# Optimization experiments

Measured on AMD Instinct MI355X. Metric: run time of the kernel, lower is better.

The kernel has to match this reference:

```python
import jax, jax.numpy as jnp
import numpy as np

N_NODES = 50000
N_EDGES = 800000
D_IN = 128
D_HID = 128
D_OUT = 128


def setup_inputs() -> dict:
    key = jax.random.key(0)
    ks = jax.random.split(key, 6)
    x = jax.random.normal(ks[0], (N_NODES, D_IN), dtype=jnp.float32)
    edge_index = jax.random.randint(ks[1], (2, N_EDGES), 0, N_NODES, dtype=jnp.int64)
    s_in = 1.0 / np.sqrt(D_IN)
    s_hid = 1.0 / np.sqrt(D_HID)
    W1 = jax.random.normal(ks[2], (D_IN, D_HID), dtype=jnp.float32) * s_in
    b1 = jnp.zeros((D_HID,), dtype=jnp.float32)
    W2 = jax.random.normal(ks[3], (D_HID, D_OUT), dtype=jnp.float32) * s_hid
    b2 = jnp.zeros((D_OUT,), dtype=jnp.float32)
    return {"x": x, "edge_index": edge_index, "W1": W1, "b1": b1, "W2": W2, "b2": b2}


def gcn_conv(x, src, dst, W, b):
    # x: [N, Din]; src/dst: [E+N] (self-loops already appended)
    N = x.shape[0]
    h = x @ W  # [N, Dout] dense transform first (PyG GCNConv order)
    deg = jnp.zeros((N,), h.dtype).at[dst].add(jnp.ones((), h.dtype))
    dinv = jax.lax.rsqrt(deg)  # deg >= 1 thanks to self-loops
    norm = dinv[src] * dinv[dst]  # [E+N] symmetric normalization
    msg = h[src] * norm[:, None]  # per-edge gathered messages
    out = jax.ops.segment_sum(msg, dst, num_segments=N)
    return out + b


def reference(x, edge_index, W1, b1, W2, b2):
    N = x.shape[0]
    loop = jnp.arange(N, dtype=edge_index.dtype)
    src = jnp.concatenate([edge_index[0], loop])
    dst = jnp.concatenate([edge_index[1], loop])
    h = jax.nn.relu(gcn_conv(x, src, dst, W1, b1))
    out = gcn_conv(h, src, dst, W2, b2)
    return out
```

## Files before the change

### kernel.cpp

```cpp
#include <hip/hip_runtime.h>

#define N_NODES 50000
#define N_EDGES 800000
#define D 128
#define NBUK 196
#define HB 128
#define EPB 6250

typedef __attribute__((ext_vector_type(8))) short bf16x8;
typedef __attribute__((ext_vector_type(4))) float f32x4;

__device__ inline unsigned short f2bf(float f) {
    unsigned u = __float_as_uint(f);
    u += 0x7fffu + ((u >> 16) & 1u);
    return (unsigned short)(u >> 16);
}
__device__ inline float bf2f(unsigned short h) {
    return __uint_as_float((unsigned)h << 16);
}

__global__ void prepw_kernel(const float* __restrict__ W1, const float* __restrict__ W2,
                             unsigned short* __restrict__ Wt) {
    int tid = blockIdx.x * 256 + threadIdx.x;
    int a = tid >> 14;
    int idx = tid & 16383;
    const float* W = a ? W2 : W1;
    float w = W[idx];
    unsigned short hi = f2bf(w);
    unsigned short lo = f2bf(w - bf2f(hi));
    int k = idx >> 7, col = idx & 127;
    int byte = (col * 128 + k) * 2;
    int swz = byte ^ (((byte >> 8) & 7) << 4);
    unsigned short* base = Wt + a * 32768;
    *(unsigned short*)((char*)base + swz) = hi;
    *(unsigned short*)((char*)(base + 16384) + swz) = lo;
}

__global__ __launch_bounds__(256) void khist_kernel(const int* __restrict__ dst,
                                                    int* __restrict__ H) {
    __shared__ int hist[NBUK];
    const int t = threadIdx.x;
    if (t < NBUK) hist[t] = 0;
    __syncthreads();
    const int e0 = blockIdx.x * EPB;
    for (int i = t; i < EPB; i += 256)
        atomicAdd(&hist[dst[e0 + i] >> 8], 1);
    __syncthreads();
    if (t < NBUK) H[blockIdx.x * NBUK + t] = hist[t];
}

__global__ __launch_bounds__(256) void kscan_kernel(const int* __restrict__ H,
                                                    int* __restrict__ B,
                                                    int* __restrict__ bbase,
                                                    int* __restrict__ bsize) {
    __shared__ int s[256];
    const int t = threadIdx.x;
    int sum = 0;
    if (t < NBUK)
        for (int blk = 0; blk < HB; ++blk) sum += H[blk * NBUK + t];
    s[t] = sum;
    __syncthreads();
    #pragma unroll
    for (int off = 1; off < 256; off <<= 1) {
        int add = (t >= off) ? s[t - off] : 0;
        __syncthreads();
        s[t] += add;
        __syncthreads();
    }
    int base = s[t] - sum;
    if (t < NBUK) {
        bbase[t] = base;
        bsize[t] = sum;
        int run = base;
        for (int blk = 0; blk < HB; ++blk) {
            B[blk * NBUK + t] = run;
            run += H[blk * NBUK + t];
        }
    }
}

__global__ __launch_bounds__(256) void kstage_kernel(const int* __restrict__ src,
                                                     const int* __restrict__ dst,
                                                     const int* __restrict__ B,
                                                     unsigned* __restrict__ stage) {
    __shared__ int cur[NBUK];
    const int t = threadIdx.x;
    if (t < NBUK) cur[t] = B[blockIdx.x * NBUK + t];
    __syncthreads();
    const int e0 = blockIdx.x * EPB;
    for (int i = t; i < EPB; i += 256) {
        int d = dst[e0 + i];
        int s = src[e0 + i];
        int pos = atomicAdd(&cur[d >> 8], 1);
        stage[pos] = (unsigned)s | ((unsigned)(d & 255) << 16);
    }
}

__global__ __launch_bounds__(256) void kfinal_kernel(const unsigned* __restrict__ stage,
                                                     const int* __restrict__ bbase,
                                                     const int* __restrict__ bsize,
                                                     int* __restrict__ cnt,
                                                     int* __restrict__ offs,
                                                     float* __restrict__ dinv,
                                                     int* __restrict__ csr) {
    __shared__ int hist[256];
    __shared__ int s[256];
    const int t = threadIdx.x;
    const int k = blockIdx.x;
    const int base = bbase[k];
    const int size = bsize[k];
    hist[t] = 0;
    __syncthreads();
    for (int i = t; i < size; i += 256)
        atomicAdd(&hist[stage[base + i] >> 16], 1);
    __syncthreads();
    int deg = hist[t];
    s[t] = deg;
    __syncthreads();
    #pragma unroll
    for (int off = 1; off < 256; off <<= 1) {
        int add = (t >= off) ? s[t - off] : 0;
        __syncthreads();
        s[t] += add;
        __syncthreads();
    }
    int excl = s[t] - deg;
    int node = k * 256 + t;
    if (node < N_NODES) {
        cnt[node] = deg;
        offs[node] = base + excl;
        dinv[node] = rsqrtf((float)deg + 1.0f);
    }
    hist[t] = base + excl;
    __syncthreads();
    for (int i = t; i < size; i += 256) {
        unsigned v = stage[base + i];
        int pos = atomicAdd(&hist[v >> 16], 1);
        csr[pos] = (int)(v & 0xffffu);
    }
}

template<bool RELU>
__global__ __launch_bounds__(256) void mfma_gemm_kernel(const float* __restrict__ A,
                                                        const unsigned short* __restrict__ Wt,
                                                        unsigned short* __restrict__ Cb,
                                                        int M) {
    __shared__ unsigned short lds[32768];
    const int tid = threadIdx.x;
    #pragma unroll
    for (int i = 0; i < 16; ++i) {
        int off = i * 4096 + tid * 16;
        *(uint4*)((char*)lds + off) = *(const uint4*)((const char*)Wt + off);
    }

    const int lane = tid & 63;
    const int wave = tid >> 6;
    const int c = lane & 15;
    const int g = lane >> 4;
    const int arow_i = blockIdx.x * 64 + wave * 16 + c;
    const bool inb = arow_i < M;
    const float* arow = A + (size_t)arow_i * D;

    bf16x8 ah[4], al[4];
    #pragma unroll
    for (int s = 0; s < 4; ++s) {
        int k0 = s * 32 + g * 8;
        float4 v0 = {0.f, 0.f, 0.f, 0.f}, v1 = {0.f, 0.f, 0.f, 0.f};
        if (inb) {
            v0 = *(const float4*)(arow + k0);
            v1 = *(const float4*)(arow + k0 + 4);
        }
        float av[8] = {v0.x, v0.y, v0.z, v0.w, v1.x, v1.y, v1.z, v1.w};
        #pragma unroll
        for (int j = 0; j < 8; ++j) {
            float f = av[j];
            if (RELU) f = fmaxf(f, 0.f);
            unsigned short h = f2bf(f);
            unsigned short l = f2bf(f - bf2f(h));
            ah[s][j] = (short)h;
            al[s][j] = (short)l;
        }
    }
    __syncthreads();

    f32x4 acc[8];
    #pragma unroll
    for (int t = 0; t < 8; ++t) { f32x4 z = {0.f, 0.f, 0.f, 0.f}; acc[t] = z; }

    const int xmask = (lane & 7) << 4;
    #pragma unroll
    for (int s = 0; s < 4; ++s) {
        int lowk = (s * 64 + g * 16) ^ xmask;
        #pragma unroll
        for (int t = 0; t < 8; ++t) {
            int off = t * 4096 + c * 256 + lowk;
            bf16x8 bh = *(const bf16x8*)((const char*)lds + off);
            bf16x8 bl = *(const bf16x8*)((const char*)lds + 32768 + off);
            acc[t] = __builtin_amdgcn_mfma_f32_16x16x32_bf16(al[s], bh, acc[t], 0, 0, 0);
            acc[t] = __builtin_amdgcn_mfma_f32_16x16x32_bf16(ah[s], bl, acc[t], 0, 0, 0);
            acc[t] = __builtin_amdgcn_mfma_f32_16x16x32_bf16(ah[s], bh, acc[t], 0, 0, 0);
        }
    }

    const int r0 = blockIdx.x * 64 + wave * 16 + g * 4;
    #pragma unroll
    for (int t = 0; t < 8; ++t) {
        #pragma unroll
        for (int r = 0; r < 4; ++r) {
            int grow = r0 + r;
            if (grow < M) Cb[(size_t)grow * D + t * 16 + c] = f2bf(acc[t][r]);
        }
    }
}

__global__ __launch_bounds__(256) void gather_kernel(const unsigned short* __restrict__ hnb,
                                                     const float* __restrict__ dinv,
                                                     const int* __restrict__ offs,
                                                     const int* __restrict__ cnt,
                                                     const int* __restrict__ csr,
                                                     const float* __restrict__ bias,
                                                     float* __restrict__ out) {
    const int wid = threadIdx.x >> 6;
    const int lane = threadIdx.x & 63;
    const int n = blockIdx.x * 4 + wid;
    if (n >= N_NODES) return;
    const int beg = offs[n];
    const int m = cnt[n];
    const int col = lane * 2;

    float ax = 0.f, ay = 0.f;
    int i = 0;
    for (; i + 4 <= m; i += 4) {
        int s0 = csr[beg + i];
        int s1 = csr[beg + i + 1];
        int s2 = csr[beg + i + 2];
        int s3 = csr[beg + i + 3];
        float w0 = dinv[s0], w1 = dinv[s1], w2 = dinv[s2], w3 = dinv[s3];
        unsigned v0 = *(const unsigned*)(hnb + (size_t)s0 * D + col);
        unsigned v1 = *(const unsigned*)(hnb + (size_t)s1 * D + col);
        unsigned v2 = *(const unsigned*)(hnb + (size_t)s2 * D + col);
        unsigned v3 = *(const unsigned*)(hnb + (size_t)s3 * D + col);
        ax = fmaf(w0, __uint_as_float(v0 << 16), ax);
        ax = fmaf(w1, __uint_as_float(v1 << 16), ax);
        ax = fmaf(w2, __uint_as_float(v2 << 16), ax);
        ax = fmaf(w3, __uint_as_float(v3 << 16), ax);
        ay = fmaf(w0, __uint_as_float(v0 & 0xffff0000u), ay);
        ay = fmaf(w1, __uint_as_float(v1 & 0xffff0000u), ay);
        ay = fmaf(w2, __uint_as_float(v2 & 0xffff0000u), ay);
        ay = fmaf(w3, __uint_as_float(v3 & 0xffff0000u), ay);
    }
    for (; i < m; ++i) {
        int s = csr[beg + i];
        float w = dinv[s];
        unsigned v = *(const unsigned*)(hnb + (size_t)s * D + col);
        ax = fmaf(w, __uint_as_float(v << 16), ax);
        ay = fmaf(w, __uint_as_float(v & 0xffff0000u), ay);
    }
    float dn = dinv[n];
    float dn2 = dn * dn;
    unsigned hv = *(const unsigned*)(hnb + (size_t)n * D + col);
    float2 bv = *(const float2*)&bias[col];
    float ox = fmaf(dn, ax, fmaf(dn2, __uint_as_float(hv << 16), bv.x));
    float oy = fmaf(dn, ay, fmaf(dn2, __uint_as_float(hv & 0xffff0000u), bv.y));
    float2 o = {ox, oy};
    *(float2*)&out[(size_t)n * D + col] = o;
}

extern "C" void kernel_launch(void* const* d_in, const int* in_sizes, int n_in,
                              void* d_out, int out_size, void* d_ws, size_t ws_size,
                              hipStream_t stream) {
    const float* x  = (const float*)d_in[0];
    const int*   ei = (const int*)d_in[1];
    const float* W1 = (const float*)d_in[2];
    const float* b1 = (const float*)d_in[3];
    const float* W2 = (const float*)d_in[4];
    const float* b2 = (const float*)d_in[5];
    float* out = (float*)d_out;

    const int* src = ei;
    const int* dst = ei + N_EDGES;

    int* wsi = (int*)d_ws;
    int*      cnt   = wsi;
    int*      offs  = cnt + 50176;
    float*    dinv  = (float*)(offs + 50176);
    int*      bbase = (int*)(dinv + 50176);
    int*      bsize = bbase + 256;
    int*      H     = bsize + 256;
    int*      B     = H + 25088;
    unsigned* stage = (unsigned*)(B + 25088);
    int*      csr   = (int*)(stage + 800000);
    unsigned short* Wt = (unsigned short*)(csr + 800000);
    unsigned short* hn = Wt + 65536;
    float* agg1 = (float*)(hn + (size_t)N_NODES * D + 64);

    const int Bt = 256;

    prepw_kernel<<<128, Bt, 0, stream>>>(W1, W2, Wt);

    khist_kernel<<<HB, Bt, 0, stream>>>(dst, H);
    kscan_kernel<<<1, Bt, 0, stream>>>(H, B, bbase, bsize);
    kstage_kernel<<<HB, Bt, 0, stream>>>(src, dst, B, stage);
    kfinal_kernel<<<NBUK, Bt, 0, stream>>>(stage, bbase, bsize, cnt, offs, dinv, csr);

    const int gemm_grid = (N_NODES + 63) / 64;
    const int gather_grid = (N_NODES + 3) / 4;

    mfma_gemm_kernel<false><<<gemm_grid, Bt, 0, stream>>>(x, Wt, hn, N_NODES);
    gather_kernel<<<gather_grid, Bt, 0, stream>>>(hn, dinv, offs, cnt, csr, b1, agg1);

    mfma_gemm_kernel<true><<<gemm_grid, Bt, 0, stream>>>(agg1, Wt + 32768, hn, N_NODES);
    gather_kernel<<<gather_grid, Bt, 0, stream>>>(hn, dinv, offs, cnt, csr, b2, out);
}
```

Before: 231.1 us.

## Merge independent kernels horizontally and deepen gather unrolling to eight edges

Merges the weight-prep and edge-histogram kernels into one launch, and runs the first GEMM in the same launch as the CSR finalisation by giving each its own block range. This removes two kernel launches and lets independent work overlap on the GPU. The gather loop is also unrolled to eight edges so more loads are in flight per wave. The fused GEMM block now declares 64 KB of shared memory, which may lower occupancy for the GEMM and the finalise blocks.

Result: faster. 212.5 us (-8.1%).

```diff
diff --git a/kernel.cpp b/kernel.cpp
--- a/kernel.cpp
+++ b/kernel.cpp
@@ -19,34 +19,38 @@
     return __uint_as_float((unsigned)h << 16);
 }
 
-__global__ void prepw_kernel(const float* __restrict__ W1, const float* __restrict__ W2,
-                             unsigned short* __restrict__ Wt) {
-    int tid = blockIdx.x * 256 + threadIdx.x;
-    int a = tid >> 14;
-    int idx = tid & 16383;
-    const float* W = a ? W2 : W1;
-    float w = W[idx];
-    unsigned short hi = f2bf(w);
-    unsigned short lo = f2bf(w - bf2f(hi));
-    int k = idx >> 7, col = idx & 127;
-    int byte = (col * 128 + k) * 2;
-    int swz = byte ^ (((byte >> 8) & 7) << 4);
-    unsigned short* base = Wt + a * 32768;
-    *(unsigned short*)((char*)base + swz) = hi;
-    *(unsigned short*)((char*)(base + 16384) + swz) = lo;
-}
-
-__global__ __launch_bounds__(256) void khist_kernel(const int* __restrict__ dst,
-                                                    int* __restrict__ H) {
+__global__ __launch_bounds__(256) void prep_hist_kernel(const float* __restrict__ W1,
+                                                        const float* __restrict__ W2,
+                                                        unsigned short* __restrict__ Wt,
+                                                        const int* __restrict__ dst,
+                                                        int* __restrict__ H) {
     __shared__ int hist[NBUK];
+    const int b = blockIdx.x;
     const int t = threadIdx.x;
-    if (t < NBUK) hist[t] = 0;
-    __syncthreads();
-    const int e0 = blockIdx.x * EPB;
-    for (int i = t; i < EPB; i += 256)
-        atomicAdd(&hist[dst[e0 + i] >> 8], 1);
-    __syncthreads();
-    if (t < NBUK) H[blockIdx.x * NBUK + t] = hist[t];
+    if (b < 128) {
+        int tid = b * 256 + t;
+        int a = tid >> 14;
+        int idx = tid & 16383;
+        const float* W = a ? W2 : W1;
+        float w = W[idx];
+        unsigned short hi = f2bf(w);
+        unsigned short lo = f2bf(w - bf2f(hi));
+        int k = idx >> 7, col = idx & 127;
+        int byte = (col * 128 + k) * 2;
+        int swz = byte ^ (((byte >> 8) & 7) << 4);
+        unsigned short* base = Wt + a * 32768;
+        *(unsigned short*)((char*)base + swz) = hi;
+        *(unsigned short*)((char*)(base + 16384) + swz) = lo;
+    } else {
+        const int blk = b - 128;
+        if (t < NBUK) hist[t] = 0;
+        __syncthreads();
+        const int e0 = blk * EPB;
+        for (int i = t; i < EPB; i += 256)
+            atomicAdd(&hist[dst[e0 + i] >> 8], 1);
+        __syncthreads();
+        if (t < NBUK) H[blk * NBUK + t] = hist[t];
+    }
 }
 
 __global__ __launch_bounds__(256) void kscan_kernel(const int* __restrict__ H,
@@ -96,55 +100,122 @@
     }
 }
 
-__global__ __launch_bounds__(256) void kfinal_kernel(const unsigned* __restrict__ stage,
-                                                     const int* __restrict__ bbase,
-                                                     const int* __restrict__ bsize,
-                                                     int* __restrict__ cnt,
-                                                     int* __restrict__ offs,
-                                                     float* __restrict__ dinv,
-                                                     int* __restrict__ csr) {
-    __shared__ int hist[256];
-    __shared__ int s[256];
-    const int t = threadIdx.x;
-    const int k = blockIdx.x;
-    const int base = bbase[k];
-    const int size = bsize[k];
-    hist[t] = 0;
-    __syncthreads();
-    for (int i = t; i < size; i += 256)
-        atomicAdd(&hist[stage[base + i] >> 16], 1);
-    __syncthreads();
-    int deg = hist[t];
-    s[t] = deg;
-    __syncthreads();
-    #pragma unroll
-    for (int off = 1; off < 256; off <<= 1) {
-        int add = (t >= off) ? s[t - off] : 0;
-        __syncthreads();
-        s[t] += add;
-        __syncthreads();
-    }
-    int excl = s[t] - deg;
-    int node = k * 256 + t;
-    if (node < N_NODES) {
-        cnt[node] = deg;
-        offs[node] = base + excl;
-        dinv[node] = rsqrtf((float)deg + 1.0f);
-    }
-    hist[t] = base + excl;
-    __syncthreads();
-    for (int i = t; i < size; i += 256) {
-        unsigned v = stage[base + i];
-        int pos = atomicAdd(&hist[v >> 16], 1);
-        csr[pos] = (int)(v & 0xffffu);
-    }
-}
-
-template<bool RELU>
-__global__ __launch_bounds__(256) void mfma_gemm_kernel(const float* __restrict__ A,
-                                                        const unsigned short* __restrict__ Wt,
-                                                        unsigned short* __restrict__ Cb,
-                                                        int M) {
+__global__ __launch_bounds__(256) void gemm1_final_kernel(
+        const float* __restrict__ A, const unsigned short* __restrict__ Wt,
+        unsigned short* __restrict__ Cb, int M, int ngemm,
+        const unsigned* __restrict__ stage, const int* __restrict__ bbase,
+        const int* __restrict__ bsize, int* __restrict__ cnt, int* __restrict__ offs,
+        float* __restrict__ dinv, int* __restrict__ csr) {
+    __shared__ char smem[65536];
+    const int tid = threadIdx.x;
+
+    if ((int)blockIdx.x < ngemm) {
+        unsigned short* lds = (unsigned short*)smem;
+        #pragma unroll
+        for (int i = 0; i < 16; ++i) {
+            int off = i * 4096 + tid * 16;
+            *(uint4*)((char*)lds + off) = *(const uint4*)((const char*)Wt + off);
+        }
+        const int lane = tid & 63;
+        const int wave = tid >> 6;
+        const int c = lane & 15;
+        const int g = lane >> 4;
+        const int arow_i = blockIdx.x * 64 + wave * 16 + c;
+        const bool inb = arow_i < M;
+        const float* arow = A + (size_t)arow_i * D;
+
+        bf16x8 ah[4], al[4];
+        #pragma unroll
+        for (int s = 0; s < 4; ++s) {
+            int k0 = s * 32 + g * 8;
+            float4 v0 = {0.f, 0.f, 0.f, 0.f}, v1 = {0.f, 0.f, 0.f, 0.f};
+            if (inb) {
+                v0 = *(const float4*)(arow + k0);
+                v1 = *(const float4*)(arow + k0 + 4);
+            }
+            float av[8] = {v0.x, v0.y, v0.z, v0.w, v1.x, v1.y, v1.z, v1.w};
+            #pragma unroll
+            for (int j = 0; j < 8; ++j) {
+                float f = av[j];
+                unsigned short h = f2bf(f);
+                unsigned short l = f2bf(f - bf2f(h));
+                ah[s][j] = (short)h;
+                al[s][j] = (short)l;
+            }
+        }
+        __syncthreads();
+
+        f32x4 acc[8];
+        #pragma unroll
+        for (int t = 0; t < 8; ++t) { f32x4 z = {0.f, 0.f, 0.f, 0.f}; acc[t] = z; }
+
+        const int xmask = (lane & 7) << 4;
+        #pragma unroll
+        for (int s = 0; s < 4; ++s) {
+            int lowk = (s * 64 + g * 16) ^ xmask;
+            #pragma unroll
+            for (int t = 0; t < 8; ++t) {
+                int off = t * 4096 + c * 256 + lowk;
+                bf16x8 bh = *(const bf16x8*)((const char*)lds + off);
+                bf16x8 bl = *(const bf16x8*)((const char*)lds + 32768 + off);
+                acc[t] = __builtin_amdgcn_mfma_f32_16x16x32_bf16(al[s], bh, acc[t], 0, 0, 0);
+                acc[t] = __builtin_amdgcn_mfma_f32_16x16x32_bf16(ah[s], bl, acc[t], 0, 0, 0);
+                acc[t] = __builtin_amdgcn_mfma_f32_16x16x32_bf16(ah[s], bh, acc[t], 0, 0, 0);
+            }
+        }
+
+        const int r0 = blockIdx.x * 64 + wave * 16 + g * 4;
+        #pragma unroll
+        for (int t = 0; t < 8; ++t) {
+            #pragma unroll
+            for (int r = 0; r < 4; ++r) {
+                int grow = r0 + r;
+                if (grow < M) Cb[(size_t)grow * D + t * 16 + c] = f2bf(acc[t][r]);
+            }
+        }
+    } else {
+        int* hist = (int*)smem;
+        int* s    = hist + 256;
+        const int t = tid;
+        const int k = blockIdx.x - ngemm;
+        const int base = bbase[k];
+        const int size = bsize[k];
+        hist[t] = 0;
+        __syncthreads();
+        for (int i = t; i < size; i += 256)
+            atomicAdd(&hist[stage[base + i] >> 16], 1);
+        __syncthreads();
+        int deg = hist[t];
+        s[t] = deg;
+        __syncthreads();
+        #pragma unroll
+        for (int off = 1; off < 256; off <<= 1) {
+            int add = (t >= off) ? s[t - off] : 0;
+            __syncthreads();
+            s[t] += add;
+            __syncthreads();
+        }
+        int excl = s[t] - deg;
+        int node = k * 256 + t;
+        if (node < N_NODES) {
+            cnt[node] = deg;
+            offs[node] = base + excl;
+            dinv[node] = rsqrtf((float)deg + 1.0f);
+        }
+        hist[t] = base + excl;
+        __syncthreads();
+        for (int i = t; i < size; i += 256) {
+            unsigned v = stage[base + i];
+            int pos = atomicAdd(&hist[v >> 16], 1);
+            csr[pos] = (int)(v & 0xffffu);
+        }
+    }
+}
+
+__global__ __launch_bounds__(256) void mfma_gemm_relu_kernel(const float* __restrict__ A,
+                                                             const unsigned short* __restrict__ Wt,
+                                                             unsigned short* __restrict__ Cb,
+                                                             int M) {
     __shared__ unsigned short lds[32768];
     const int tid = threadIdx.x;
     #pragma unroll
@@ -152,7 +223,6 @@
         int off = i * 4096 + tid * 16;
         *(uint4*)((char*)lds + off) = *(const uint4*)((const char*)Wt + off);
     }
-
     const int lane = tid & 63;
     const int wave = tid >> 6;
     const int c = lane & 15;
@@ -173,8 +243,7 @@
         float av[8] = {v0.x, v0.y, v0.z, v0.w, v1.x, v1.y, v1.z, v1.w};
         #pragma unroll
         for (int j = 0; j < 8; ++j) {
-            float f = av[j];
-            if (RELU) f = fmaxf(f, 0.f);
+            float f = fmaxf(av[j], 0.f);
             unsigned short h = f2bf(f);
             unsigned short l = f2bf(f - bf2f(h));
             ah[s][j] = (short)h;
@@ -230,24 +299,34 @@
 
     float ax = 0.f, ay = 0.f;
     int i = 0;
+    for (; i + 8 <= m; i += 8) {
+        int sidx[8];
+        #pragma unroll
+        for (int j = 0; j < 8; ++j) sidx[j] = csr[beg + i + j];
+        float w[8];
+        unsigned v[8];
+        #pragma unroll
+        for (int j = 0; j < 8; ++j) {
+            w[j] = dinv[sidx[j]];
+            v[j] = *(const unsigned*)(hnb + (size_t)sidx[j] * D + col);
+        }
+        #pragma unroll
+        for (int j = 0; j < 8; ++j) {
+            ax = fmaf(w[j], __uint_as_float(v[j] << 16), ax);
+            ay = fmaf(w[j], __uint_as_float(v[j] & 0xffff0000u), ay);
+        }
+    }
     for (; i + 4 <= m; i += 4) {
-        int s0 = csr[beg + i];
-        int s1 = csr[beg + i + 1];
-        int s2 = csr[beg + i + 2];
-        int s3 = csr[beg + i + 3];
-        float w0 = dinv[s0], w1 = dinv[s1], w2 = dinv[s2], w3 = dinv[s3];
-        unsigned v0 = *(const unsigned*)(hnb + (size_t)s0 * D + col);
-        unsigned v1 = *(const unsigned*)(hnb + (size_t)s1 * D + col);
-        unsigned v2 = *(const unsigned*)(hnb + (size_t)s2 * D + col);
-        unsigned v3 = *(const unsigned*)(hnb + (size_t)s3 * D + col);
-        ax = fmaf(w0, __uint_as_float(v0 << 16), ax);
-        ax = fmaf(w1, __uint_as_float(v1 << 16), ax);
-        ax = fmaf(w2, __uint_as_float(v2 << 16), ax);
-        ax = fmaf(w3, __uint_as_float(v3 << 16), ax);
-        ay = fmaf(w0, __uint_as_float(v0 & 0xffff0000u), ay);
-        ay = fmaf(w1, __uint_as_float(v1 & 0xffff0000u), ay);
-        ay = fmaf(w2, __uint_as_float(v2 & 0xffff0000u), ay);
-        ay = fmaf(w3, __uint_as_float(v3 & 0xffff0000u), ay);
+        int sidx[4];
+        #pragma unroll
+        for (int j = 0; j < 4; ++j) sidx[j] = csr[beg + i + j];
+        #pragma unroll
+        for (int j = 0; j < 4; ++j) {
+            float w = dinv[sidx[j]];
+            unsigned v = *(const unsigned*)(hnb + (size_t)sidx[j] * D + col);
+            ax = fmaf(w, __uint_as_float(v << 16), ax);
+            ay = fmaf(w, __uint_as_float(v & 0xffff0000u), ay);
+        }
     }
     for (; i < m; ++i) {
         int s = csr[beg + i];
@@ -295,20 +374,19 @@
     float* agg1 = (float*)(hn + (size_t)N_NODES * D + 64);
 
     const int Bt = 256;
-
-    prepw_kernel<<<128, Bt, 0, stream>>>(W1, W2, Wt);
-
-    khist_kernel<<<HB, Bt, 0, stream>>>(dst, H);
+    const int gemm_grid = (N_NODES + 63) / 64;
+    const int gather_grid = (N_NODES + 3) / 4;
+
+    prep_hist_kernel<<<256, Bt, 0, stream>>>(W1, W2, Wt, dst, H);
     kscan_kernel<<<1, Bt, 0, stream>>>(H, B, bbase, bsize);
     kstage_kernel<<<HB, Bt, 0, stream>>>(src, dst, B, stage);
-    kfinal_kernel<<<NBUK, Bt, 0, stream>>>(stage, bbase, bsize, cnt, offs, dinv, csr);
-
-    const int gemm_grid = (N_NODES + 63) / 64;
-    const int gather_grid = (N_NODES + 3) / 4;
-
-    mfma_gemm_kernel<false><<<gemm_grid, Bt, 0, stream>>>(x, Wt, hn, N_NODES);
+
+    gemm1_final_kernel<<<gemm_grid + NBUK, Bt, 0, stream>>>(
+        x, Wt, hn, N_NODES, gemm_grid,
+        stage, bbase, bsize, cnt, offs, dinv, csr);
+
     gather_kernel<<<gather_grid, Bt, 0, stream>>>(hn, dinv, offs, cnt, csr, b1, agg1);
 
-    mfma_gemm_kernel<true><<<gemm_grid, Bt, 0, stream>>>(agg1, Wt + 32768, hn, N_NODES);
+    mfma_gemm_relu_kernel<<<gemm_grid, Bt, 0, stream>>>(agg1, Wt + 32768, hn, N_NODES);
     gather_kernel<<<gather_grid, Bt, 0, stream>>>(hn, dinv, offs, cnt, csr, b2, out);
 }
```
